# Kernel optimization log

Hardware: AMD Instinct MI355X
Metric: run time of the kernel (lower is better)

Reference implementation:

```python
import jax, jax.numpy as jnp
import numpy as np

IN_DIM = 64
QK_DIM = IN_DIM // 8
SHAPE_X = (2, IN_DIM, 20, 20, 20)


def setup_inputs() -> dict:
    key = jax.random.key(0)
    ks = jax.random.split(key, 8)
    C, Cq = IN_DIM, QK_DIM
    s_in = 1.0 / np.sqrt(C)
    return {
        "x": jax.random.normal(ks[0], SHAPE_X, dtype=jnp.float32),
        "wq": jax.random.normal(ks[1], (Cq, C), dtype=jnp.float32) * s_in,
        "bq": jax.random.normal(ks[2], (Cq,), dtype=jnp.float32) * 0.01,
        "wk": jax.random.normal(ks[3], (Cq, C), dtype=jnp.float32) * s_in,
        "bk": jax.random.normal(ks[4], (Cq,), dtype=jnp.float32) * 0.01,
        "wv": jax.random.normal(ks[5], (C, C), dtype=jnp.float32) * s_in,
        "bv": jax.random.normal(ks[6], (C,), dtype=jnp.float32) * 0.01,
        "gamma": jax.random.normal(ks[7], (1,), dtype=jnp.float32),
    }


def reference(x, wq, bq, wk, bk, wv, bv, gamma):
    B, C, D, H, W = x.shape
    N = D * H * W
    xf = x.reshape(B, C, N)                                   # [B, C, N]
    # 1x1x1 convs == per-voxel channel linear maps
    q = jnp.einsum('qc,bcn->bnq', wq, xf) + bq                # [B, N, Cq]
    k = jnp.einsum('qc,bcn->bqn', wk, xf) + bk[:, None]       # [B, Cq, N]
    energy = jnp.einsum('bnq,bqm->bnm', q, k)                 # [B, N, N]
    attn = jax.nn.softmax(energy, axis=-1)                    # rows sum to 1
    v = jnp.einsum('vc,bcn->bvn', wv, xf) + bv[:, None]       # [B, C, N]
    # out = bmm(v, attn^T): out[b,c,m] = sum_n v[b,c,n] * attn[b,m,n]
    out = jnp.einsum('bvn,bmn->bvm', v, attn)                 # [B, C, N]
    out = out.reshape(B, C, D, H, W)
    return gamma * out + x
```

## Files before the change

kernel.cpp:

```cpp
#include <hip/hip_runtime.h>
#include <math.h>

#define BATCH  2
#define NVOX   8000
#define MT     32
#define KT     64
#define NTILES 125
#define QTILES 250
#define LOG2E  1.44269504f
#define MSTAT  32.0f

typedef float  f32x16 __attribute__((ext_vector_type(16)));
typedef __bf16 bf16x8 __attribute__((ext_vector_type(8)));
typedef unsigned short u16x8 __attribute__((ext_vector_type(8)));

__device__ __forceinline__ unsigned short f2bf(float f) {
    return __builtin_bit_cast(unsigned short, (__bf16)f);
}
__device__ __forceinline__ unsigned int packbf(float lo, float hi) {
    unsigned int r;
    asm("v_cvt_pk_bf16_f32 %0, %1, %2" : "=v"(r) : "v"(lo), "v"(hi));
    return r;
}
__device__ __forceinline__ float fexp2(float x) {
    return __builtin_amdgcn_exp2f(x);
}


__global__ __launch_bounds__(192) void qkv_kernel(
    const float* __restrict__ x,
    const float* __restrict__ wq, const float* __restrict__ bq,
    const float* __restrict__ wk, const float* __restrict__ bk,
    const float* __restrict__ wv, const float* __restrict__ bv,
    unsigned short* __restrict__ qws, unsigned short* __restrict__ kws,
    unsigned short* __restrict__ vws)
{
    __shared__ __align__(16) unsigned short st[88 * 40];
    const int t = threadIdx.x, lane = t & 63, ot = t >> 6;
    const int l31 = lane & 31, h = lane >> 5;
    const int blk = blockIdx.x, b = blk / 250, v0 = (blk % 250) * 32;
    const int n = v0 + l31;

    const int o = ot * 32 + l31;
    const float* wsrc;
    float scale = 1.0f;
    if (o < 8)       { wsrc = wq + o * 64; scale = LOG2E; }
    else if (o < 16) { wsrc = wk + (o - 8) * 64; }
    else             { wsrc = wv + ((o - 16) & 63) * 64; }

    bf16x8 Ah[4], Al[4];
#pragma unroll
    for (int cc = 0; cc < 4; ++cc) {
        float4 w0 = *(const float4*)(wsrc + cc * 16 + 8 * h);
        float4 w1 = *(const float4*)(wsrc + cc * 16 + 8 * h + 4);
        float wf[8] = { w0.x, w0.y, w0.z, w0.w, w1.x, w1.y, w1.z, w1.w };
        unsigned short hh[8], ll[8];
#pragma unroll
        for (int j = 0; j < 8; ++j) {
            float wv_ = wf[j] * scale;
            __bf16 hb = (__bf16)wv_;
            hh[j] = __builtin_bit_cast(unsigned short, hb);
            ll[j] = f2bf(wv_ - (float)hb);
        }
        Ah[cc] = __builtin_bit_cast(bf16x8, *(u16x8*)hh);
        Al[cc] = __builtin_bit_cast(bf16x8, *(u16x8*)ll);
    }

    bf16x8 Bhi[4], Blo[4];
    const float* xb = x + (size_t)b * 64 * NVOX + n;
#pragma unroll
    for (int cc = 0; cc < 4; ++cc) {
        unsigned short bh[8], bl[8];
#pragma unroll
        for (int j = 0; j < 8; ++j) {
            float xf = xb[(size_t)(cc * 16 + 8 * h + j) * NVOX];
            __bf16 xh = (__bf16)xf;
            bh[j] = __builtin_bit_cast(unsigned short, xh);
            bl[j] = f2bf(xf - (float)xh);
        }
        Bhi[cc] = __builtin_bit_cast(bf16x8, *(u16x8*)bh);
        Blo[cc] = __builtin_bit_cast(bf16x8, *(u16x8*)bl);
    }

    f32x16 acc;
#pragma unroll
    for (int r = 0; r < 16; ++r) acc[r] = 0.0f;
#pragma unroll
    for (int cc = 0; cc < 4; ++cc) {
        acc = __builtin_amdgcn_mfma_f32_32x32x16_bf16(Ah[cc], Bhi[cc], acc, 0, 0, 0);
        acc = __builtin_amdgcn_mfma_f32_32x32x16_bf16(Al[cc], Bhi[cc], acc, 0, 0, 0);
        acc = __builtin_amdgcn_mfma_f32_32x32x16_bf16(Ah[cc], Blo[cc], acc, 0, 0, 0);
    }

#pragma unroll
    for (int r = 0; r < 16; ++r) {
        int oo = ot * 32 + (r & 3) + 8 * (r >> 2) + 4 * h;
        if (oo >= 80) continue;
        float bias = (oo < 8) ? bq[oo] * LOG2E : (oo < 16) ? bk[oo - 8] : bv[oo - 16];
        float v = acc[r] + bias;
        if (oo < 8) {
            __bf16 hb = (__bf16)v;
            st[oo * 40 + l31]        = __builtin_bit_cast(unsigned short, hb);
            st[(80 + oo) * 40 + l31] = f2bf(v - (float)hb);
        } else {
            st[oo * 40 + l31] = f2bf(v);
        }
    }
    __syncthreads();

    for (int idx = t; idx < 256; idx += 192) {
        int ch = idx >> 2, q = idx & 3;
        int T = v0 >> 6;
        int off = (v0 & 63) + q * 8;
        int s2 = off >> 4, p = (off >> 3) & 1;
        int cg = ch >> 5, c31 = ch & 31;
        size_t dst = (size_t)(b * 125 + T) * 4096 + s2 * 1024 + cg * 512
                   + p * 256 + c31 * 8;
        *(uint4*)(vws + dst) = *(const uint4*)&st[(16 + ch) * 40 + q * 8];
    }
    if (t >= 128) {
        int i = t - 128, vox = i >> 1, half = i & 1;
        int rbase = half ? 80 : 0;
        unsigned short g[8];
#pragma unroll
        for (int r = 0; r < 8; ++r) g[r] = st[(rbase + r) * 40 + vox];
        *(uint4*)(qws + (size_t)(b * NVOX + v0 + vox) * 16 + half * 8) = *(uint4*)g;
    } else if (t >= 96) {
        int vox = t - 96;
        unsigned short g[8];
#pragma unroll
        for (int r = 0; r < 8; ++r) g[r] = st[(8 + r) * 40 + vox];
        *(uint4*)(kws + (size_t)(b * NVOX + v0 + vox) * 8) = *(uint4*)g;
    }
}

__global__ __launch_bounds__(512, 1) void attn_kernel(
    const unsigned short* __restrict__ qws, const unsigned short* __restrict__ kws,
    const unsigned short* __restrict__ vws, const float* __restrict__ x,
    const float* __restrict__ gamma, float* __restrict__ out)
{
    __shared__ float smem_f[8704];
    float* l_sh = smem_f + 8192;

    const int blk = blockIdx.x, b = blk / QTILES, m0 = (blk % QTILES) * MT;
    const int t = threadIdx.x, lane = t & 63, w = t >> 6;
    const int l31 = lane & 31, h = lane >> 5;

    const bf16x8 qf = __builtin_bit_cast(bf16x8,
        *(const u16x8*)(qws + (size_t)(b * NVOX + m0 + l31) * 16 + h * 8));

    const unsigned short* ksrc = kws + (size_t)b * NVOX * 8;
    const unsigned short* vbase = vws + (size_t)b * 512000 + h * 256 + l31 * 8;

    f32x16 acc0, acc1, zro;
#pragma unroll
    for (int r = 0; r < 16; ++r) { acc0[r] = 0.0f; acc1[r] = 0.0f; zro[r] = 0.0f; }
    float sA = 0.0f, sB = 0.0f, sC = 0.0f, sD = 0.0f;

    uint4 va0[4], va1[4];
    uint4 pf[4];
    bf16x8 kf0c = __builtin_bit_cast(bf16x8, *(const u16x8*)(ksrc + (size_t)(w * KT + l31) * 8));
    bf16x8 kf1c = __builtin_bit_cast(bf16x8, *(const u16x8*)(ksrc + (size_t)(w * KT + 32 + l31) * 8));
    bool havePrev = false;

#pragma unroll 1
    for (int S = 0; S < 16; ++S) {
        const int T = w + 8 * S;
        if (T < NTILES) {
            const int Tn = T + 8;

            bf16x8 kf0n = kf0c, kf1n = kf1c;
            if (Tn < NTILES) {
                const int nn = Tn * KT;
                kf0n = __builtin_bit_cast(bf16x8, *(const u16x8*)(ksrc + (size_t)(nn + l31) * 8));
                kf1n = __builtin_bit_cast(bf16x8, *(const u16x8*)(ksrc + (size_t)(nn + 32 + l31) * 8));
            }

            f32x16 E0 = __builtin_amdgcn_mfma_f32_32x32x16_bf16(kf0c, qf, zro, 0, 0, 0);
            f32x16 E1 = __builtin_amdgcn_mfma_f32_32x32x16_bf16(kf1c, qf, zro, 0, 0, 0);
            kf0c = kf0n; kf1c = kf1n;

            unsigned int pk0[8], q0s[8], pk1[8], q1s[8];
#pragma unroll
            for (int g = 0; g < 8; ++g) {
                float pa = fexp2(E0[2 * g] - MSTAT);
                float pb = fexp2(E0[2 * g + 1] - MSTAT);
                sA += pa; sB += pb;
                pk0[g] = packbf(pa, pb);
            }
#pragma unroll
            for (int g = 0; g < 8; ++g) {
                float pa = fexp2(E1[2 * g] - MSTAT);
                float pb = fexp2(E1[2 * g + 1] - MSTAT);
                sC += pa; sD += pb;
                pk1[g] = packbf(pa, pb);
            }
#pragma unroll
            for (int g = 0; g < 8; ++g)
                q0s[g] = (unsigned int)__shfl_xor((int)pk0[g], 32, 64);
#pragma unroll
            for (int g = 0; g < 8; ++g)
                q1s[g] = (unsigned int)__shfl_xor((int)pk1[g], 32, 64);

            if (havePrev) {
#pragma unroll
                for (int s2 = 0; s2 < 4; ++s2)
                    acc0 = __builtin_amdgcn_mfma_f32_32x32x16_bf16(
                        __builtin_bit_cast(bf16x8, va0[s2]),
                        __builtin_bit_cast(bf16x8, pf[s2]), acc0, 0, 0, 0);
#pragma unroll
                for (int s2 = 0; s2 < 4; ++s2)
                    acc1 = __builtin_amdgcn_mfma_f32_32x32x16_bf16(
                        __builtin_bit_cast(bf16x8, va1[s2]),
                        __builtin_bit_cast(bf16x8, pf[s2]), acc1, 0, 0, 0);
            }

            {
                const unsigned short* vt = vbase + (size_t)T * 4096;
#pragma unroll
                for (int s2 = 0; s2 < 4; ++s2) {
                    va0[s2] = *(const uint4*)(vt + s2 * 1024);
                    va1[s2] = *(const uint4*)(vt + s2 * 1024 + 512);
                }
            }

#pragma unroll
            for (int s2 = 0; s2 < 2; ++s2) {
                const int ba = 4 * s2;
                pf[s2].x = h ? q0s[ba + 2] : pk0[ba];
                pf[s2].y = h ? q0s[ba + 3] : pk0[ba + 1];
                pf[s2].z = h ? pk0[ba + 2] : q0s[ba];
                pf[s2].w = h ? pk0[ba + 3] : q0s[ba + 1];
            }
#pragma unroll
            for (int s2 = 2; s2 < 4; ++s2) {
                const int ba = 4 * (s2 - 2);
                pf[s2].x = h ? q1s[ba + 2] : pk1[ba];
                pf[s2].y = h ? q1s[ba + 3] : pk1[ba + 1];
                pf[s2].z = h ? pk1[ba + 2] : q1s[ba];
                pf[s2].w = h ? pk1[ba + 3] : q1s[ba + 1];
            }
            havePrev = true;
        }
    }

#pragma unroll
    for (int s2 = 0; s2 < 4; ++s2)
        acc0 = __builtin_amdgcn_mfma_f32_32x32x16_bf16(
            __builtin_bit_cast(bf16x8, va0[s2]),
            __builtin_bit_cast(bf16x8, pf[s2]), acc0, 0, 0, 0);
#pragma unroll
    for (int s2 = 0; s2 < 4; ++s2)
        acc1 = __builtin_amdgcn_mfma_f32_32x32x16_bf16(
            __builtin_bit_cast(bf16x8, va1[s2]),
            __builtin_bit_cast(bf16x8, pf[s2]), acc1, 0, 0, 0);

    l_sh[w * 64 + lane] = (sA + sB) + (sC + sD);
    float* mw = smem_f;
    auto wr = [&](int srcw) {
#pragma unroll
        for (int r4 = 0; r4 < 4; ++r4) {
            *(float4*)&mw[((size_t)(srcw * 2 + 0) * 64 + lane) * 16 + 4 * r4] =
                make_float4(acc0[4*r4], acc0[4*r4+1], acc0[4*r4+2], acc0[4*r4+3]);
            *(float4*)&mw[((size_t)(srcw * 2 + 1) * 64 + lane) * 16 + 4 * r4] =
                make_float4(acc1[4*r4], acc1[4*r4+1], acc1[4*r4+2], acc1[4*r4+3]);
        }
    };
    auto rd = [&](int srcw) {
#pragma unroll
        for (int r4 = 0; r4 < 4; ++r4) {
            float4 a = *(const float4*)&mw[((size_t)(srcw * 2 + 0) * 64 + lane) * 16 + 4 * r4];
            float4 c = *(const float4*)&mw[((size_t)(srcw * 2 + 1) * 64 + lane) * 16 + 4 * r4];
            acc0[4*r4]   += a.x; acc0[4*r4+1] += a.y; acc0[4*r4+2] += a.z; acc0[4*r4+3] += a.w;
            acc1[4*r4]   += c.x; acc1[4*r4+1] += c.y; acc1[4*r4+2] += c.z; acc1[4*r4+3] += c.w;
        }
    };
    if (w >= 4) wr(w - 4);
    __syncthreads();
    if (w < 4) rd(w);
    __syncthreads();
    if (w >= 2 && w < 4) wr(w - 2);
    __syncthreads();
    if (w < 2) rd(w);
    __syncthreads();
    if (w == 1) wr(0);
    __syncthreads();
    if (w == 0) {
        rd(0);
        float l_tot = 0.0f;
#pragma unroll
        for (int ww = 0; ww < 8; ++ww)
            l_tot += l_sh[ww * 64 + l31] + l_sh[ww * 64 + 32 + l31];
        const float inv = 1.0f / l_tot;
        const float g = gamma[0];
#pragma unroll
        for (int r = 0; r < 16; ++r) {
            int c = (r & 3) + 8 * (r >> 2) + 4 * h;
            size_t i0 = ((size_t)b * 64 + c) * NVOX + m0 + l31;
            size_t i1 = ((size_t)b * 64 + c + 32) * NVOX + m0 + l31;
            out[i0] = g * (acc0[r] * inv) + x[i0];
            out[i1] = g * (acc1[r] * inv) + x[i1];
        }
    }
}

extern "C" void kernel_launch(void* const* d_in, const int* in_sizes, int n_in,
                              void* d_out, int out_size, void* d_ws, size_t ws_size,
                              hipStream_t stream) {
    const float* x     = (const float*)d_in[0];
    const float* wq    = (const float*)d_in[1];
    const float* bq    = (const float*)d_in[2];
    const float* wk    = (const float*)d_in[3];
    const float* bk    = (const float*)d_in[4];
    const float* wv    = (const float*)d_in[5];
    const float* bv    = (const float*)d_in[6];
    const float* gamma = (const float*)d_in[7];
    float* out = (float*)d_out;

    unsigned short* qws = (unsigned short*)d_ws;
    unsigned short* kws = qws + (size_t)BATCH * NVOX * 16;
    unsigned short* vws = kws + (size_t)BATCH * NVOX * 8;

    qkv_kernel<<<500, 192, 0, stream>>>(x, wq, bq, wk, bk, wv, bv, qws, kws, vws);
    attn_kernel<<<BATCH * QTILES, 512, 0, stream>>>(qws, kws, vws, x, gamma, out);
}
```

Baseline: 115.4 us.

## Fold softmax shift into MFMA accumulator and swap lanes with permlane32

Seeds the QK^T MFMA accumulator with -MSTAT so the constant subtraction before each exp2 disappears. The 16 ds_bpermute-style shuffles plus select logic that rebuild the P operand are replaced with 8 v_permlane32_swap instructions. The exp/pack stage moves after the PV MFMAs and V loads so the PV matrix work can overlap it, and those MFMAs run under raised s_setprio. The changes cut VALU and LDS-crossbar work in the inner loop but rely on permlane32_swap semantics matching the old half-wave exchange.

```diff
diff --git a/kernel.cpp b/kernel.cpp
--- a/kernel.cpp
+++ b/kernel.cpp
@@ -24,6 +24,9 @@
 }
 __device__ __forceinline__ float fexp2(float x) {
     return __builtin_amdgcn_exp2f(x);
+}
+__device__ __forceinline__ void plswap(unsigned &a, unsigned &b) {
+    asm("v_permlane32_swap_b32 %0, %1" : "+v"(a), "+v"(b));
 }
 
 
@@ -152,9 +155,9 @@
     const unsigned short* ksrc = kws + (size_t)b * NVOX * 8;
     const unsigned short* vbase = vws + (size_t)b * 512000 + h * 256 + l31 * 8;
 
-    f32x16 acc0, acc1, zro;
-#pragma unroll
-    for (int r = 0; r < 16; ++r) { acc0[r] = 0.0f; acc1[r] = 0.0f; zro[r] = 0.0f; }
+    f32x16 acc0, acc1, mC;
+#pragma unroll
+    for (int r = 0; r < 16; ++r) { acc0[r] = 0.0f; acc1[r] = 0.0f; mC[r] = -MSTAT; }
     float sA = 0.0f, sB = 0.0f, sC = 0.0f, sD = 0.0f;
 
     uint4 va0[4], va1[4];
@@ -176,33 +179,12 @@
                 kf1n = __builtin_bit_cast(bf16x8, *(const u16x8*)(ksrc + (size_t)(nn + 32 + l31) * 8));
             }
 
-            f32x16 E0 = __builtin_amdgcn_mfma_f32_32x32x16_bf16(kf0c, qf, zro, 0, 0, 0);
-            f32x16 E1 = __builtin_amdgcn_mfma_f32_32x32x16_bf16(kf1c, qf, zro, 0, 0, 0);
+            f32x16 E0 = __builtin_amdgcn_mfma_f32_32x32x16_bf16(kf0c, qf, mC, 0, 0, 0);
+            f32x16 E1 = __builtin_amdgcn_mfma_f32_32x32x16_bf16(kf1c, qf, mC, 0, 0, 0);
             kf0c = kf0n; kf1c = kf1n;
 
-            unsigned int pk0[8], q0s[8], pk1[8], q1s[8];
-#pragma unroll
-            for (int g = 0; g < 8; ++g) {
-                float pa = fexp2(E0[2 * g] - MSTAT);
-                float pb = fexp2(E0[2 * g + 1] - MSTAT);
-                sA += pa; sB += pb;
-                pk0[g] = packbf(pa, pb);
-            }
-#pragma unroll
-            for (int g = 0; g < 8; ++g) {
-                float pa = fexp2(E1[2 * g] - MSTAT);
-                float pb = fexp2(E1[2 * g + 1] - MSTAT);
-                sC += pa; sD += pb;
-                pk1[g] = packbf(pa, pb);
-            }
-#pragma unroll
-            for (int g = 0; g < 8; ++g)
-                q0s[g] = (unsigned int)__shfl_xor((int)pk0[g], 32, 64);
-#pragma unroll
-            for (int g = 0; g < 8; ++g)
-                q1s[g] = (unsigned int)__shfl_xor((int)pk1[g], 32, 64);
-
             if (havePrev) {
+                __builtin_amdgcn_s_setprio(1);
 #pragma unroll
                 for (int s2 = 0; s2 < 4; ++s2)
                     acc0 = __builtin_amdgcn_mfma_f32_32x32x16_bf16(
@@ -213,6 +195,7 @@
                     acc1 = __builtin_amdgcn_mfma_f32_32x32x16_bf16(
                         __builtin_bit_cast(bf16x8, va1[s2]),
                         __builtin_bit_cast(bf16x8, pf[s2]), acc1, 0, 0, 0);
+                __builtin_amdgcn_s_setprio(0);
             }
 
             {
@@ -224,26 +207,38 @@
                 }
             }
 
-#pragma unroll
-            for (int s2 = 0; s2 < 2; ++s2) {
-                const int ba = 4 * s2;
-                pf[s2].x = h ? q0s[ba + 2] : pk0[ba];
-                pf[s2].y = h ? q0s[ba + 3] : pk0[ba + 1];
-                pf[s2].z = h ? pk0[ba + 2] : q0s[ba];
-                pf[s2].w = h ? pk0[ba + 3] : q0s[ba + 1];
-            }
-#pragma unroll
-            for (int s2 = 2; s2 < 4; ++s2) {
-                const int ba = 4 * (s2 - 2);
-                pf[s2].x = h ? q1s[ba + 2] : pk1[ba];
-                pf[s2].y = h ? q1s[ba + 3] : pk1[ba + 1];
-                pf[s2].z = h ? pk1[ba + 2] : q1s[ba];
-                pf[s2].w = h ? pk1[ba + 3] : q1s[ba + 1];
+            unsigned int pk0[8], pk1[8];
+#pragma unroll
+            for (int g = 0; g < 8; ++g) {
+                float pa = fexp2(E0[2 * g]);
+                float pb = fexp2(E0[2 * g + 1]);
+                sA += pa; sB += pb;
+                pk0[g] = packbf(pa, pb);
+            }
+#pragma unroll
+            for (int g = 0; g < 8; ++g) {
+                float pa = fexp2(E1[2 * g]);
+                float pb = fexp2(E1[2 * g + 1]);
+                sC += pa; sD += pb;
+                pk1[g] = packbf(pa, pb);
+            }
+
+            {
+                unsigned a0, b0;
+                a0 = pk0[0]; b0 = pk0[2]; plswap(a0, b0); pf[0].x = a0; pf[0].z = b0;
+                a0 = pk0[1]; b0 = pk0[3]; plswap(a0, b0); pf[0].y = a0; pf[0].w = b0;
+                a0 = pk0[4]; b0 = pk0[6]; plswap(a0, b0); pf[1].x = a0; pf[1].z = b0;
+                a0 = pk0[5]; b0 = pk0[7]; plswap(a0, b0); pf[1].y = a0; pf[1].w = b0;
+                a0 = pk1[0]; b0 = pk1[2]; plswap(a0, b0); pf[2].x = a0; pf[2].z = b0;
+                a0 = pk1[1]; b0 = pk1[3]; plswap(a0, b0); pf[2].y = a0; pf[2].w = b0;
+                a0 = pk1[4]; b0 = pk1[6]; plswap(a0, b0); pf[3].x = a0; pf[3].z = b0;
+                a0 = pk1[5]; b0 = pk1[7]; plswap(a0, b0); pf[3].y = a0; pf[3].w = b0;
             }
             havePrev = true;
         }
     }
 
+    __builtin_amdgcn_s_setprio(1);
 #pragma unroll
     for (int s2 = 0; s2 < 4; ++s2)
         acc0 = __builtin_amdgcn_mfma_f32_32x32x16_bf16(
@@ -254,6 +249,7 @@
         acc1 = __builtin_amdgcn_mfma_f32_32x32x16_bf16(
             __builtin_bit_cast(bf16x8, va1[s2]),
             __builtin_bit_cast(bf16x8, pf[s2]), acc1, 0, 0, 0);
+    __builtin_amdgcn_s_setprio(0);
 
     l_sh[w * 64 + lane] = (sA + sB) + (sC + sD);
     float* mw = smem_f;
```

After: 110.3 us. 4.4% less time.
